# Performance work log

Hardware: AMD Instinct MI355X
Metric: run time of the kernel (lower is better)

Reference implementation:

```python
import jax, jax.numpy as jnp
import numpy as np

HIDDEN = 512
VOCAB = 50000
SEQ = 4096


def setup_inputs() -> dict:
    key = jax.random.key(0)
    ks = jax.random.split(key, 8)
    s = 1.0 / np.sqrt(HIDDEN)
    return {
        "x": jax.random.randint(ks[0], (1, SEQ), 0, VOCAB, dtype=jnp.int64),
        "target": jax.random.uniform(ks[1], (1, 1), dtype=jnp.float32),
        "emb": jax.random.normal(ks[2], (VOCAB, HIDDEN), dtype=jnp.float32),
        "w_ih": jax.random.uniform(ks[3], (3 * HIDDEN, HIDDEN), minval=-s, maxval=s, dtype=jnp.float32),
        "w_hh": jax.random.uniform(ks[4], (3 * HIDDEN, HIDDEN), minval=-s, maxval=s, dtype=jnp.float32),
        "b_ih": jax.random.uniform(ks[5], (3 * HIDDEN,), minval=-s, maxval=s, dtype=jnp.float32),
        "b_hh": jax.random.uniform(ks[6], (3 * HIDDEN,), minval=-s, maxval=s, dtype=jnp.float32),
        "dec_w": jax.random.uniform(ks[7], (1, HIDDEN), minval=-s, maxval=s, dtype=jnp.float32),
        "dec_b": jnp.zeros((1,), dtype=jnp.float32),
    }


def reference(x, target, emb, w_ih, w_hh, b_ih, b_hh, dec_w, dec_b):
    H = emb.shape[1]
    # embedding lookup for whole sequence (dropout in eval mode = identity)
    xe = emb[x[0]]                       # [S, H]
    # precompute input-side gate projections for all timesteps
    gx = xe @ w_ih.T + b_ih              # [S, 3H]

    def step(h, gx_t):
        gh = h @ w_hh.T + b_hh           # [3H]
        r = jax.nn.sigmoid(gx_t[:H] + gh[:H])
        z = jax.nn.sigmoid(gx_t[H:2 * H] + gh[H:2 * H])
        n = jnp.tanh(gx_t[2 * H:] + r * gh[2 * H:])
        h_new = (1.0 - z) * n + z * h
        return h_new, None

    h0 = jnp.zeros((H,), dtype=xe.dtype)
    hT, _ = jax.lax.scan(step, h0, gx)   # final hidden state [H]

    # decoder logit, then sigmoid + BCE (stable log-sigmoid form)
    logit = hT @ dec_w[0] + dec_b[0]     # scalar
    t = target[0, 0]
    loss = -(t * jax.nn.log_sigmoid(logit) + (1.0 - t) * jax.nn.log_sigmoid(-logit))
    return loss
```

## Files before the change

### kernel.cpp

```cpp
#include <hip/hip_runtime.h>

constexpr int S   = 4096;
constexpr int H   = 512;
constexpr int G3  = 1536;
constexpr int NWG = 32;

__device__ inline uint4 ld4_mall(const void* p) {
    uint4 v;
    asm volatile("global_load_dwordx4 %0, %1, off sc0 sc1\n\ts_waitcnt vmcnt(0)"
                 : "=v"(v) : "v"(p) : "memory");
    return v;
}

__device__ inline void barrier_lds() {
    __builtin_amdgcn_sched_barrier(0);
    asm volatile("s_waitcnt lgkmcnt(0)" ::: "memory");
    __builtin_amdgcn_s_barrier();
    __builtin_amdgcn_sched_barrier(0);
}

__global__ __launch_bounds__(256) void gemm_gx(
    const int* __restrict__ x, const float* __restrict__ emb,
    const float* __restrict__ w_ih, const float* __restrict__ b_ih,
    float* __restrict__ gx)
{
    __shared__ alignas(16) float As[128][36];
    __shared__ alignas(16) float Bs[32][132];

    const int tid  = threadIdx.x;
    const int row0 = (blockIdx.x / 12) * 128;
    const int col0 = (blockIdx.x % 12) * 128;
    const int tx   = tid & 15;
    const int ty   = tid >> 4;

    float acc[8][8] = {};

    for (int k0 = 0; k0 < H; k0 += 32) {
        #pragma unroll
        for (int p = 0; p < 4; ++p) {
            const int rl = (tid >> 3) + 32 * p;
            const int kk = (tid & 7) * 4;
            const int xi = x[row0 + rl];
            const float4 va = *reinterpret_cast<const float4*>(
                emb + (size_t)xi * H + k0 + kk);
            *reinterpret_cast<float4*>(&As[rl][kk]) = va;

            const float4 vb = *reinterpret_cast<const float4*>(
                w_ih + (size_t)(col0 + rl) * H + k0 + kk);
            Bs[kk + 0][rl] = vb.x; Bs[kk + 1][rl] = vb.y;
            Bs[kk + 2][rl] = vb.z; Bs[kk + 3][rl] = vb.w;
        }
        __syncthreads();

        #pragma unroll
        for (int kk = 0; kk < 32; ++kk) {
            float a[8], b[8];
            #pragma unroll
            for (int q = 0; q < 4; ++q) {
                a[q]     = As[ty * 4 + q][kk];
                a[4 + q] = As[ty * 4 + 64 + q][kk];
            }
            const float4 b0 = *reinterpret_cast<const float4*>(&Bs[kk][tx * 4]);
            const float4 b1 = *reinterpret_cast<const float4*>(&Bs[kk][tx * 4 + 64]);
            b[0]=b0.x; b[1]=b0.y; b[2]=b0.z; b[3]=b0.w;
            b[4]=b1.x; b[5]=b1.y; b[6]=b1.z; b[7]=b1.w;
            #pragma unroll
            for (int ri = 0; ri < 8; ++ri)
                #pragma unroll
                for (int ci = 0; ci < 8; ++ci)
                    acc[ri][ci] = fmaf(a[ri], b[ci], acc[ri][ci]);
        }
        __syncthreads();
    }

    float bi[8];
    #pragma unroll
    for (int q = 0; q < 4; ++q) {
        bi[q]     = b_ih[col0 + tx * 4 + q];
        bi[4 + q] = b_ih[col0 + tx * 4 + 64 + q];
    }
    #pragma unroll
    for (int ri = 0; ri < 8; ++ri) {
        const int rr = row0 + ty * 4 + (ri & 3) + ((ri >> 2) << 6);
        float4 o0, o1;
        o0.x = acc[ri][0] + bi[0]; o0.y = acc[ri][1] + bi[1];
        o0.z = acc[ri][2] + bi[2]; o0.w = acc[ri][3] + bi[3];
        o1.x = acc[ri][4] + bi[4]; o1.y = acc[ri][5] + bi[5];
        o1.z = acc[ri][6] + bi[6]; o1.w = acc[ri][7] + bi[7];
        *reinterpret_cast<float4*>(gx + (size_t)rr * G3 + col0 + tx * 4)      = o0;
        *reinterpret_cast<float4*>(gx + (size_t)rr * G3 + col0 + tx * 4 + 64) = o1;
    }
}

__global__ __launch_bounds__(256, 1) void gru_scan(
    const float* __restrict__ gx,
    const float* __restrict__ w_hh,
    const float* __restrict__ b_hh,
    const float* __restrict__ dec_w,
    const float* __restrict__ dec_b,
    const float* __restrict__ target,
    unsigned long long* __restrict__ hbuf,
    float* __restrict__ out)
{
    __shared__ float h_lds[H];

    const int k   = blockIdx.x;
    const int tid = threadIdx.x;
    const int l   = tid & 15;
    const int g   = tid >> 4;
    const int i   = k * 16 + g;

    float4 wr[8], wz[8], wn[8];
    #pragma unroll
    for (int j = 0; j < 8; ++j) {
        const int c = 4 * l + 64 * j;
        wr[j] = *reinterpret_cast<const float4*>(w_hh + (size_t)i * H + c);
        wz[j] = *reinterpret_cast<const float4*>(w_hh + (size_t)(H + i) * H + c);
        wn[j] = *reinterpret_cast<const float4*>(w_hh + (size_t)(2 * H + i) * H + c);
    }
    const float bhr = b_hh[i], bhz = b_hh[H + i], bhn = b_hh[2 * H + i];

    float gxr = 0.f, gxz = 0.f, gxn = 0.f;
    if (l == 0) { gxr = gx[i]; gxz = gx[H + i]; gxn = gx[2 * H + i]; }

    const int e0 = 2 * tid, e1 = 2 * tid + 1;

    for (int s = 0; s < S; ++s) {
        if (s == 0) {
            h_lds[e0] = 0.f; h_lds[e1] = 0.f;
        } else {
            const unsigned tg = (unsigned)s;
            const void* src =
                (const char*)(hbuf + (size_t)(s & 1) * H) + 16 * (size_t)tid;
            uint4 v = ld4_mall(src);
            while (!(v.y == tg && v.w == tg)) {
                v = ld4_mall(src);
            }
            h_lds[e0] = __uint_as_float(v.x);
            h_lds[e1] = __uint_as_float(v.z);
        }
        barrier_lds();

        const float hp = h_lds[i];

        float ar = 0.f, az = 0.f, an = 0.f;
        #pragma unroll
        for (int j = 0; j < 8; ++j) {
            const float4 hv =
                *reinterpret_cast<const float4*>(&h_lds[64 * j + 4 * l]);
            ar = fmaf(wr[j].x, hv.x, fmaf(wr[j].y, hv.y,
                 fmaf(wr[j].z, hv.z, fmaf(wr[j].w, hv.w, ar))));
            az = fmaf(wz[j].x, hv.x, fmaf(wz[j].y, hv.y,
                 fmaf(wz[j].z, hv.z, fmaf(wz[j].w, hv.w, az))));
            an = fmaf(wn[j].x, hv.x, fmaf(wn[j].y, hv.y,
                 fmaf(wn[j].z, hv.z, fmaf(wn[j].w, hv.w, an))));
        }
        #pragma unroll
        for (int m = 8; m >= 1; m >>= 1) {
            ar += __shfl_xor(ar, m);
            az += __shfl_xor(az, m);
            an += __shfl_xor(an, m);
        }

        if (l == 0) {
            const float r  = 1.f / (1.f + __expf(-(gxr + ar + bhr)));
            const float z  = 1.f / (1.f + __expf(-(gxz + az + bhz)));
            const float nn = tanhf(gxn + r * (an + bhn));
            const float hnew = (1.f - z) * nn + z * hp;
            const unsigned long long pv =
                ((unsigned long long)(unsigned)(s + 1) << 32) |
                (unsigned long long)__float_as_uint(hnew);
            __hip_atomic_store(hbuf + (size_t)((s + 1) & 1) * H + i, pv,
                               __ATOMIC_RELAXED, __HIP_MEMORY_SCOPE_AGENT);
            const int sn = (s + 1 < S) ? (s + 1) : s;
            gxr = gx[(size_t)sn * G3 + i];
            gxz = gx[(size_t)sn * G3 + H + i];
            gxn = gx[(size_t)sn * G3 + 2 * H + i];
        }
        barrier_lds();
    }

    if (k == 0) {
        const unsigned tg = (unsigned)S;
        const void* src = (const char*)hbuf + 16 * (size_t)tid;
        uint4 v = ld4_mall(src);
        while (!(v.y == tg && v.w == tg)) {
            v = ld4_mall(src);
        }
        h_lds[e0] = __uint_as_float(v.x);
        h_lds[e1] = __uint_as_float(v.z);
        __syncthreads();

        if (tid < 64) {
            float p = 0.f;
            #pragma unroll
            for (int j = 0; j < 8; ++j)
                p = fmaf(h_lds[tid + 64 * j], dec_w[tid + 64 * j], p);
            #pragma unroll
            for (int m = 32; m >= 1; m >>= 1) p += __shfl_xor(p, m);
            if (tid == 0) {
                const float xl = p + dec_b[0];
                const float t  = target[0];
                const float loss = fmaxf(xl, 0.f) - xl * t +
                                   log1pf(__expf(-fabsf(xl)));
                out[0] = loss;
            }
        }
    }
}

extern "C" void kernel_launch(void* const* d_in, const int* in_sizes, int n_in,
                              void* d_out, int out_size, void* d_ws, size_t ws_size,
                              hipStream_t stream) {
    const int*   x      = (const int*)d_in[0];
    const float* target = (const float*)d_in[1];
    const float* emb    = (const float*)d_in[2];
    const float* w_ih   = (const float*)d_in[3];
    const float* w_hh   = (const float*)d_in[4];
    const float* b_ih   = (const float*)d_in[5];
    const float* b_hh   = (const float*)d_in[6];
    const float* dec_w  = (const float*)d_in[7];
    const float* dec_b  = (const float*)d_in[8];
    float*       out    = (float*)d_out;

    float* gx = (float*)d_ws;
    unsigned long long* hbuf =
        (unsigned long long*)((char*)d_ws + (size_t)S * G3 * sizeof(float));

    hipMemsetAsync(hbuf, 0, 2 * H * sizeof(unsigned long long), stream);

    gemm_gx<<<dim3(32 * 12), dim3(256), 0, stream>>>(x, emb, w_ih, b_ih, gx);
    gru_scan<<<dim3(NWG), dim3(256), 0, stream>>>(gx, w_hh, b_hh, dec_w, dec_b,
                                                  target, hbuf, out);
}
```

Measured before the change: 7.934 ms.

## Drop workgroup barriers by giving each wave its own hidden-state copy

Result: slower. 12.51 ms (+57.7%).

```diff
diff --git a/kernel.cpp b/kernel.cpp
--- a/kernel.cpp
+++ b/kernel.cpp
@@ -4,20 +4,7 @@
 constexpr int H   = 512;
 constexpr int G3  = 1536;
 constexpr int NWG = 32;
-
-__device__ inline uint4 ld4_mall(const void* p) {
-    uint4 v;
-    asm volatile("global_load_dwordx4 %0, %1, off sc0 sc1\n\ts_waitcnt vmcnt(0)"
-                 : "=v"(v) : "v"(p) : "memory");
-    return v;
-}
-
-__device__ inline void barrier_lds() {
-    __builtin_amdgcn_sched_barrier(0);
-    asm volatile("s_waitcnt lgkmcnt(0)" ::: "memory");
-    __builtin_amdgcn_s_barrier();
-    __builtin_amdgcn_sched_barrier(0);
-}
+constexpr int GXW = 32;
 
 __global__ __launch_bounds__(256) void gemm_gx(
     const int* __restrict__ x, const float* __restrict__ emb,
@@ -102,13 +89,18 @@
     unsigned long long* __restrict__ hbuf,
     float* __restrict__ out)
 {
-    __shared__ float h_lds[H];
-
-    const int k   = blockIdx.x;
-    const int tid = threadIdx.x;
-    const int l   = tid & 15;
-    const int g   = tid >> 4;
-    const int i   = k * 16 + g;
+    __shared__ alignas(16) float hw[4][H];
+    __shared__ alignas(16) float gxw[4][GXW * 12];
+
+    const int tid  = threadIdx.x;
+    const int wv   = tid >> 6;
+    const int lane = tid & 63;
+    const int k    = blockIdx.x;
+    const int g    = tid >> 4;
+    const int l    = tid & 15;
+    const int r    = g & 3;
+    const int i    = k * 16 + g;
+    const int row_base = k * 16 + (wv << 2);
 
     float4 wr[8], wz[8], wn[8];
     #pragma unroll
@@ -120,34 +112,67 @@
     }
     const float bhr = b_hh[i], bhz = b_hh[H + i], bhn = b_hh[2 * H + i];
 
-    float gxr = 0.f, gxz = 0.f, gxn = 0.f;
-    if (l == 0) { gxr = gx[i]; gxz = gx[H + i]; gxn = gx[2 * H + i]; }
-
-    const int e0 = 2 * tid, e1 = 2 * tid + 1;
+    float* hl  = hw[wv];
+    float* gxl = gxw[wv];
 
     for (int s = 0; s < S; ++s) {
         if (s == 0) {
-            h_lds[e0] = 0.f; h_lds[e1] = 0.f;
+            const float4 z4 = make_float4(0.f, 0.f, 0.f, 0.f);
+            *reinterpret_cast<float4*>(&hl[8 * lane])     = z4;
+            *reinterpret_cast<float4*>(&hl[8 * lane + 4]) = z4;
         } else {
             const unsigned tg = (unsigned)s;
-            const void* src =
-                (const char*)(hbuf + (size_t)(s & 1) * H) + 16 * (size_t)tid;
-            uint4 v = ld4_mall(src);
-            while (!(v.y == tg && v.w == tg)) {
-                v = ld4_mall(src);
+            const char* base =
+                (const char*)(hbuf + (size_t)(s & 1) * H) + 64 * (size_t)lane;
+            uint4 a, b, c, d;
+            while (true) {
+                asm volatile(
+                    "global_load_dwordx4 %0, %4, off sc0 sc1\n\t"
+                    "global_load_dwordx4 %1, %5, off sc0 sc1\n\t"
+                    "global_load_dwordx4 %2, %6, off sc0 sc1\n\t"
+                    "global_load_dwordx4 %3, %7, off sc0 sc1\n\t"
+                    "s_waitcnt vmcnt(0)"
+                    : "=&v"(a), "=&v"(b), "=&v"(c), "=&v"(d)
+                    : "v"(base), "v"(base + 16), "v"(base + 32), "v"(base + 48)
+                    : "memory");
+                if (a.y == tg && a.w == tg && b.y == tg && b.w == tg &&
+                    c.y == tg && c.w == tg && d.y == tg && d.w == tg) break;
             }
-            h_lds[e0] = __uint_as_float(v.x);
-            h_lds[e1] = __uint_as_float(v.z);
-        }
-        barrier_lds();
-
-        const float hp = h_lds[i];
+            float4 v0, v1;
+            v0.x = __uint_as_float(a.x); v0.y = __uint_as_float(a.z);
+            v0.z = __uint_as_float(b.x); v0.w = __uint_as_float(b.z);
+            v1.x = __uint_as_float(c.x); v1.y = __uint_as_float(c.z);
+            v1.z = __uint_as_float(d.x); v1.w = __uint_as_float(d.z);
+            *reinterpret_cast<float4*>(&hl[8 * lane])     = v0;
+            *reinterpret_cast<float4*>(&hl[8 * lane + 4]) = v1;
+        }
+
+        if ((s & (GXW - 1)) == 0) {
+            float tmp[6];
+            #pragma unroll
+            for (int m = 0; m < 6; ++m) {
+                const int idx = lane + 64 * m;
+                const int tr  = idx / 12;
+                const int rem = idx % 12;
+                const int q   = rem >> 2;
+                const int rr  = rem & 3;
+                tmp[m] = gx[(size_t)(s + tr) * G3 + q * H + row_base + rr];
+            }
+            #pragma unroll
+            for (int m = 0; m < 6; ++m) gxl[lane + 64 * m] = tmp[m];
+        }
+
+        __builtin_amdgcn_sched_barrier(0);
+        asm volatile("s_waitcnt lgkmcnt(0)" ::: "memory");
+        __builtin_amdgcn_sched_barrier(0);
+
+        const float hp = hl[i];
 
         float ar = 0.f, az = 0.f, an = 0.f;
         #pragma unroll
         for (int j = 0; j < 8; ++j) {
             const float4 hv =
-                *reinterpret_cast<const float4*>(&h_lds[64 * j + 4 * l]);
+                *reinterpret_cast<const float4*>(&hl[64 * j + 4 * l]);
             ar = fmaf(wr[j].x, hv.x, fmaf(wr[j].y, hv.y,
                  fmaf(wr[j].z, hv.z, fmaf(wr[j].w, hv.w, ar))));
             az = fmaf(wz[j].x, hv.x, fmaf(wz[j].y, hv.y,
@@ -163,48 +188,54 @@
         }
 
         if (l == 0) {
-            const float r  = 1.f / (1.f + __expf(-(gxr + ar + bhr)));
-            const float z  = 1.f / (1.f + __expf(-(gxz + az + bhz)));
-            const float nn = tanhf(gxn + r * (an + bhn));
-            const float hnew = (1.f - z) * nn + z * hp;
+            const int sl = s & (GXW - 1);
+            const float gxr = gxl[sl * 12 + r];
+            const float gxz = gxl[sl * 12 + 4 + r];
+            const float gxn = gxl[sl * 12 + 8 + r];
+            const float rr  = 1.f / (1.f + __expf(-(gxr + ar + bhr)));
+            const float zz  = 1.f / (1.f + __expf(-(gxz + az + bhz)));
+            const float nn  = tanhf(gxn + rr * (an + bhn));
+            const float hnew = (1.f - zz) * nn + zz * hp;
             const unsigned long long pv =
                 ((unsigned long long)(unsigned)(s + 1) << 32) |
                 (unsigned long long)__float_as_uint(hnew);
             __hip_atomic_store(hbuf + (size_t)((s + 1) & 1) * H + i, pv,
                                __ATOMIC_RELAXED, __HIP_MEMORY_SCOPE_AGENT);
-            const int sn = (s + 1 < S) ? (s + 1) : s;
-            gxr = gx[(size_t)sn * G3 + i];
-            gxz = gx[(size_t)sn * G3 + H + i];
-            gxn = gx[(size_t)sn * G3 + 2 * H + i];
-        }
-        barrier_lds();
-    }
-
-    if (k == 0) {
+        }
+    }
+
+    if (k == 0 && wv == 0) {
         const unsigned tg = (unsigned)S;
-        const void* src = (const char*)hbuf + 16 * (size_t)tid;
-        uint4 v = ld4_mall(src);
-        while (!(v.y == tg && v.w == tg)) {
-            v = ld4_mall(src);
-        }
-        h_lds[e0] = __uint_as_float(v.x);
-        h_lds[e1] = __uint_as_float(v.z);
-        __syncthreads();
-
-        if (tid < 64) {
-            float p = 0.f;
-            #pragma unroll
-            for (int j = 0; j < 8; ++j)
-                p = fmaf(h_lds[tid + 64 * j], dec_w[tid + 64 * j], p);
-            #pragma unroll
-            for (int m = 32; m >= 1; m >>= 1) p += __shfl_xor(p, m);
-            if (tid == 0) {
-                const float xl = p + dec_b[0];
-                const float t  = target[0];
-                const float loss = fmaxf(xl, 0.f) - xl * t +
-                                   log1pf(__expf(-fabsf(xl)));
-                out[0] = loss;
-            }
+        const char* base = (const char*)hbuf + 64 * (size_t)lane;
+        uint4 a, b, c, d;
+        while (true) {
+            asm volatile(
+                "global_load_dwordx4 %0, %4, off sc0 sc1\n\t"
+                "global_load_dwordx4 %1, %5, off sc0 sc1\n\t"
+                "global_load_dwordx4 %2, %6, off sc0 sc1\n\t"
+                "global_load_dwordx4 %3, %7, off sc0 sc1\n\t"
+                "s_waitcnt vmcnt(0)"
+                : "=&v"(a), "=&v"(b), "=&v"(c), "=&v"(d)
+                : "v"(base), "v"(base + 16), "v"(base + 32), "v"(base + 48)
+                : "memory");
+            if (a.y == tg && a.w == tg && b.y == tg && b.w == tg &&
+                c.y == tg && c.w == tg && d.y == tg && d.w == tg) break;
+        }
+        const float h0 = __uint_as_float(a.x), h1 = __uint_as_float(a.z);
+        const float h2 = __uint_as_float(b.x), h3 = __uint_as_float(b.z);
+        const float h4 = __uint_as_float(c.x), h5 = __uint_as_float(c.z);
+        const float h6 = __uint_as_float(d.x), h7 = __uint_as_float(d.z);
+        const float* dw = dec_w + 8 * lane;
+        float p = h0 * dw[0] + h1 * dw[1] + h2 * dw[2] + h3 * dw[3] +
+                  h4 * dw[4] + h5 * dw[5] + h6 * dw[6] + h7 * dw[7];
+        #pragma unroll
+        for (int m = 32; m >= 1; m >>= 1) p += __shfl_xor(p, m);
+        if (lane == 0) {
+            const float xl = p + dec_b[0];
+            const float t  = target[0];
+            const float loss = fmaxf(xl, 0.f) - xl * t +
+                               log1pf(__expf(-fabsf(xl)));
+            out[0] = loss;
         }
     }
 }
```

## Halve scan workgroups to 16 with 512 threads and prefetch next-step gates

Applied to the files above, without the earlier changes.

New measurement: 7.191 ms. -9.4%, faster.

```diff
diff --git a/kernel.cpp b/kernel.cpp
--- a/kernel.cpp
+++ b/kernel.cpp
@@ -3,11 +3,11 @@
 constexpr int S   = 4096;
 constexpr int H   = 512;
 constexpr int G3  = 1536;
-constexpr int NWG = 32;
-
-__device__ inline uint4 ld4_mall(const void* p) {
-    uint4 v;
-    asm volatile("global_load_dwordx4 %0, %1, off sc0 sc1\n\ts_waitcnt vmcnt(0)"
+constexpr int NWG = 16;
+
+__device__ inline unsigned long long ld2_mall(const void* p) {
+    unsigned long long v;
+    asm volatile("global_load_dwordx2 %0, %1, off sc0 sc1\n\ts_waitcnt vmcnt(0)"
                  : "=v"(v) : "v"(p) : "memory");
     return v;
 }
@@ -92,7 +92,7 @@
     }
 }
 
-__global__ __launch_bounds__(256, 1) void gru_scan(
+__global__ __launch_bounds__(512, 1) void gru_scan(
     const float* __restrict__ gx,
     const float* __restrict__ w_hh,
     const float* __restrict__ b_hh,
@@ -108,7 +108,7 @@
     const int tid = threadIdx.x;
     const int l   = tid & 15;
     const int g   = tid >> 4;
-    const int i   = k * 16 + g;
+    const int i   = k * 32 + g;
 
     float4 wr[8], wz[8], wn[8];
     #pragma unroll
@@ -120,75 +120,75 @@
     }
     const float bhr = b_hh[i], bhz = b_hh[H + i], bhn = b_hh[2 * H + i];
 
-    float gxr = 0.f, gxz = 0.f, gxn = 0.f;
-    if (l == 0) { gxr = gx[i]; gxz = gx[H + i]; gxn = gx[2 * H + i]; }
-
-    const int e0 = 2 * tid, e1 = 2 * tid + 1;
-
-    for (int s = 0; s < S; ++s) {
-        if (s == 0) {
-            h_lds[e0] = 0.f; h_lds[e1] = 0.f;
-        } else {
-            const unsigned tg = (unsigned)s;
-            const void* src =
-                (const char*)(hbuf + (size_t)(s & 1) * H) + 16 * (size_t)tid;
-            uint4 v = ld4_mall(src);
-            while (!(v.y == tg && v.w == tg)) {
-                v = ld4_mall(src);
-            }
-            h_lds[e0] = __uint_as_float(v.x);
-            h_lds[e1] = __uint_as_float(v.z);
-        }
-        barrier_lds();
-
-        const float hp = h_lds[i];
-
-        float ar = 0.f, az = 0.f, an = 0.f;
-        #pragma unroll
-        for (int j = 0; j < 8; ++j) {
-            const float4 hv =
-                *reinterpret_cast<const float4*>(&h_lds[64 * j + 4 * l]);
-            ar = fmaf(wr[j].x, hv.x, fmaf(wr[j].y, hv.y,
-                 fmaf(wr[j].z, hv.z, fmaf(wr[j].w, hv.w, ar))));
-            az = fmaf(wz[j].x, hv.x, fmaf(wz[j].y, hv.y,
-                 fmaf(wz[j].z, hv.z, fmaf(wz[j].w, hv.w, az))));
-            an = fmaf(wn[j].x, hv.x, fmaf(wn[j].y, hv.y,
-                 fmaf(wn[j].z, hv.z, fmaf(wn[j].w, hv.w, an))));
-        }
-        #pragma unroll
-        for (int m = 8; m >= 1; m >>= 1) {
-            ar += __shfl_xor(ar, m);
-            az += __shfl_xor(az, m);
-            an += __shfl_xor(an, m);
-        }
-
-        if (l == 0) {
-            const float r  = 1.f / (1.f + __expf(-(gxr + ar + bhr)));
-            const float z  = 1.f / (1.f + __expf(-(gxz + az + bhz)));
-            const float nn = tanhf(gxn + r * (an + bhn));
-            const float hnew = (1.f - z) * nn + z * hp;
-            const unsigned long long pv =
-                ((unsigned long long)(unsigned)(s + 1) << 32) |
-                (unsigned long long)__float_as_uint(hnew);
-            __hip_atomic_store(hbuf + (size_t)((s + 1) & 1) * H + i, pv,
-                               __ATOMIC_RELAXED, __HIP_MEMORY_SCOPE_AGENT);
-            const int sn = (s + 1 < S) ? (s + 1) : s;
-            gxr = gx[(size_t)sn * G3 + i];
-            gxz = gx[(size_t)sn * G3 + H + i];
-            gxn = gx[(size_t)sn * G3 + 2 * H + i];
-        }
-        barrier_lds();
-    }
+    float gxrA = 0.f, gxzA = 0.f, gxnA = 0.f;
+    float gxrB = 0.f, gxzB = 0.f, gxnB = 0.f;
+    if (l == 0) { gxrA = gx[i]; gxzA = gx[H + i]; gxnA = gx[2 * H + i]; }
+
+#define GRU_STEP(S_, GR_, GZ_, GN_, GRN_, GZN_, GNN_)                         \
+    {                                                                          \
+        const int s_ = (S_);                                                   \
+        if (s_ == 0) {                                                         \
+            h_lds[tid] = 0.f;                                                  \
+        } else {                                                               \
+            const unsigned tg_ = (unsigned)s_;                                 \
+            const unsigned long long* src_ =                                   \
+                hbuf + (size_t)(s_ & 1) * H + tid;                             \
+            unsigned long long v_ = ld2_mall(src_);                            \
+            while ((unsigned)(v_ >> 32) != tg_) v_ = ld2_mall(src_);           \
+            h_lds[tid] = __uint_as_float((unsigned)v_);                        \
+        }                                                                      \
+        if (l == 0) {         \
+            const int sn_ = (s_ + 1 < S) ? (s_ + 1) : (S - 1);                 \
+            GRN_ = gx[(size_t)sn_ * G3 + i];                                   \
+            GZN_ = gx[(size_t)sn_ * G3 + H + i];                               \
+            GNN_ = gx[(size_t)sn_ * G3 + 2 * H + i];                           \
+        }                                                                      \
+        barrier_lds();                                                         \
+        const float hp_ = h_lds[i];                                            \
+        float ar = 0.f, az = 0.f, an = 0.f;                                    \
+        _Pragma("unroll")                                                      \
+        for (int j = 0; j < 8; ++j) {                                          \
+            const float4 hv =                                                  \
+                *reinterpret_cast<const float4*>(&h_lds[64 * j + 4 * l]);      \
+            ar = fmaf(wr[j].x, hv.x, fmaf(wr[j].y, hv.y,                       \
+                 fmaf(wr[j].z, hv.z, fmaf(wr[j].w, hv.w, ar))));               \
+            az = fmaf(wz[j].x, hv.x, fmaf(wz[j].y, hv.y,                       \
+                 fmaf(wz[j].z, hv.z, fmaf(wz[j].w, hv.w, az))));               \
+            an = fmaf(wn[j].x, hv.x, fmaf(wn[j].y, hv.y,                       \
+                 fmaf(wn[j].z, hv.z, fmaf(wn[j].w, hv.w, an))));               \
+        }                                                                      \
+        _Pragma("unroll")                                                      \
+        for (int m = 8; m >= 1; m >>= 1) {                                     \
+            ar += __shfl_xor(ar, m);                                           \
+            az += __shfl_xor(az, m);                                           \
+            an += __shfl_xor(an, m);                                           \
+        }                                                                      \
+        if (l == 0) {                                                          \
+            const float r_  = 1.f / (1.f + __expf(-(GR_ + ar + bhr)));         \
+            const float z_  = 1.f / (1.f + __expf(-(GZ_ + az + bhz)));         \
+            const float nn_ = tanhf(GN_ + r_ * (an + bhn));                    \
+            const float hnew_ = (1.f - z_) * nn_ + z_ * hp_;                   \
+            const unsigned long long pv_ =                                     \
+                ((unsigned long long)(unsigned)(s_ + 1) << 32) |               \
+                (unsigned long long)__float_as_uint(hnew_);                    \
+            __hip_atomic_store(hbuf + (size_t)((s_ + 1) & 1) * H + i, pv_,     \
+                               __ATOMIC_RELAXED, __HIP_MEMORY_SCOPE_AGENT);    \
+        }                                                                      \
+        barrier_lds();                                                         \
+    }
+
+    for (int s = 0; s < S; s += 2) {
+        GRU_STEP(s,     gxrA, gxzA, gxnA, gxrB, gxzB, gxnB);
+        GRU_STEP(s + 1, gxrB, gxzB, gxnB, gxrA, gxzA, gxnA);
+    }
+#undef GRU_STEP
 
     if (k == 0) {
         const unsigned tg = (unsigned)S;
-        const void* src = (const char*)hbuf + 16 * (size_t)tid;
-        uint4 v = ld4_mall(src);
-        while (!(v.y == tg && v.w == tg)) {
-            v = ld4_mall(src);
-        }
-        h_lds[e0] = __uint_as_float(v.x);
-        h_lds[e1] = __uint_as_float(v.z);
+        const unsigned long long* src = hbuf + tid;
+        unsigned long long v = ld2_mall(src);
+        while ((unsigned)(v >> 32) != tg) v = ld2_mall(src);
+        h_lds[tid] = __uint_as_float((unsigned)v);
         __syncthreads();
 
         if (tid < 64) {
@@ -230,6 +230,6 @@
     hipMemsetAsync(hbuf, 0, 2 * H * sizeof(unsigned long long), stream);
 
     gemm_gx<<<dim3(32 * 12), dim3(256), 0, stream>>>(x, emb, w_ih, b_ih, gx);
-    gru_scan<<<dim3(NWG), dim3(256), 0, stream>>>(gx, w_hh, b_hh, dec_w, dec_b,
+    gru_scan<<<dim3(NWG), dim3(512), 0, stream>>>(gx, w_hh, b_hh, dec_w, dec_b,
                                                   target, hbuf, out);
 }
```
